# Kernel optimization log

Hardware: AMD Instinct MI355X
Metric: run time of the kernel (lower is better)

## Reference

```python
import jax, jax.numpy as jnp
import numpy as np
import math

MH_C = 2.0 / (math.sqrt(3.0) * math.pi ** 0.25)  # mexican hat normalization

def setup_inputs() -> dict:
    key = jax.random.key(0)
    ks = jax.random.split(key, 4)
    B, O, I, H, W = 4, 32, 32, 128, 128
    x = jax.random.normal(ks[0], (B, I, H, W), dtype=jnp.float32)
    scale_param = jnp.ones((1, O, I, 1, 1), dtype=jnp.float32)
    translation_param = jax.random.normal(ks[1], (1, O, I, 1, 1), dtype=jnp.float32)
    wavelet_conv_w = jax.random.normal(ks[2], (O, I, 3, 3), dtype=jnp.float32) * (1.0 / math.sqrt(I * 9))
    final_conv_w = jax.random.normal(ks[3], (O, O, 1, 1), dtype=jnp.float32) * (1.0 / math.sqrt(O))
    return {"x": x, "scale_param": scale_param, "translation_param": translation_param,
            "wavelet_conv_w": wavelet_conv_w, "final_conv_w": final_conv_w}

def reference(x, scale_param, translation_param, wavelet_conv_w, final_conv_w):
    # x: (B, I, H, W) -> scaled: (B, O, I, H, W)
    sx = (x[:, None] - translation_param) / scale_param
    # mexican hat wavelet, fused elementwise
    wt = MH_C * ((sx * sx - 1.0) * jnp.exp(-0.5 * sx * sx))
    B, O, I, H, W = wt.shape
    # The per-out-channel loop of Conv2d(I,1,k) is exactly a grouped conv with O groups
    wt = wt.reshape(B, O * I, H, W)
    y = jax.lax.conv_general_dilated(
        wt, wavelet_conv_w,
        window_strides=(1, 1), padding=[(1, 1), (1, 1)],
        feature_group_count=O,
        dimension_numbers=("NCHW", "OIHW", "NCHW"))  # (B, O, H, W)
    # final 1x1 conv = channel mix
    out = jnp.einsum("oc,bchw->bohw", final_conv_w[:, :, 0, 0], y)
    return out
```

## Files before the change

kernel.cpp:

```cpp
#include <hip/hip_runtime.h>
#include <math.h>


#define RSTRIP 8

typedef float v2f __attribute__((ext_vector_type(2)));

static __device__ __forceinline__ v2f vfma(float w, v2f a, v2f c) {
  return __builtin_elementwise_fma(a, (v2f){w, w}, c);
}
static __device__ __forceinline__ float bperm(int addr, float v) {
  return __int_as_float(__builtin_amdgcn_ds_bpermute(addr, __float_as_int(v)));
}

#define LDROW(base, r) (*(const v2f*)((base) + (size_t)(min(max((r), 0), 127)) * 128))

__global__ __launch_bounds__(256) void wavelet_grouped_conv(
    const float* __restrict__ x,
    const float* __restrict__ scale,
    const float* __restrict__ trans,
    const float* __restrict__ wconv,
    float* __restrict__ y,
    float mhc)
{
  const int tid   = threadIdx.x;
  const int lane  = tid & 63;
  const int iq    = tid >> 6;
  const int strip = blockIdx.x;
  const int o     = blockIdx.y;
  const int b     = blockIdx.z;
  const int r0    = strip * RSTRIP;
  const int c0    = lane << 1;

  const int a_up = ((lane + 63) & 63) << 2;
  const int a_dn = ((lane +  1) & 63) << 2;
  const bool lane0  = (lane == 0);
  const bool lane63 = (lane == 63);

  const float rvm1 = (r0 > 0)       ? 1.f : 0.f;
  const float rv8  = (r0 + 8 < 128) ? 1.f : 0.f;

  const float NHL2E = -0.72134752044448170f;

  v2f TL[RSTRIP], TC[RSTRIP], TR[RSTRIP];
#pragma unroll
  for (int r = 0; r < RSTRIP; ++r) {
    TL[r] = (v2f){0.f, 0.f}; TC[r] = (v2f){0.f, 0.f}; TR[r] = (v2f){0.f, 0.f};
  }

  const float* xb = x + (size_t)b * 32 * 128 * 128;

#pragma unroll 1
  for (int ii = 0; ii < 8; ++ii) {
    const int i0 = iq * 8 + ii;
    const int oi = __builtin_amdgcn_readfirstlane(o * 32 + i0);
    const float rs  = 1.0f / scale[oi];
    const float trs = trans[oi] * rs;
    const float* wp = wconv + oi * 9;
    const float w00 = wp[0], w01 = wp[1], w02 = wp[2];
    const float w10 = wp[3], w11 = wp[4], w12 = wp[5];
    const float w20 = wp[6], w21 = wp[7], w22 = wp[8];
    const float* base = xb + (size_t)i0 * 128 * 128 + c0;

    v2f xa = LDROW(base, r0 - 1);
    v2f xbv = LDROW(base, r0);

#pragma unroll
    for (int j = 0; j < RSTRIP + 2; ++j) {
      const v2f xc = LDROW(base, r0 + j + 1);
      const float rv = (j == 0) ? rvm1 : (j == RSTRIP + 1) ? rv8 : 1.f;
      const v2f sx = __builtin_elementwise_fma(xa, (v2f){rs, rs},
                                               (v2f){-trs, -trs});
      const v2f u  = sx * sx;
      v2f e;
      e.x = __builtin_amdgcn_exp2f(u.x * NHL2E);
      e.y = __builtin_amdgcn_exp2f(u.y * NHL2E);
      v2f p = __builtin_elementwise_fma(u, (v2f){mhc, mhc},
                                        (v2f){-mhc, -mhc}) * e;
      p = p * (v2f){rv, rv};

      if (j <= RSTRIP - 1) {
        TL[j] = vfma(w00, p, TL[j]);
        TC[j] = vfma(w01, p, TC[j]);
        TR[j] = vfma(w02, p, TR[j]);
      }
      if (j >= 1 && j <= RSTRIP) {
        TL[j-1] = vfma(w10, p, TL[j-1]);
        TC[j-1] = vfma(w11, p, TC[j-1]);
        TR[j-1] = vfma(w12, p, TR[j-1]);
      }
      if (j >= 2) {
        TL[j-2] = vfma(w20, p, TL[j-2]);
        TC[j-2] = vfma(w21, p, TC[j-2]);
        TR[j-2] = vfma(w22, p, TR[j-2]);
      }
      xa = xbv; xbv = xc;
    }
  }

  v2f acc[RSTRIP];
#pragma unroll
  for (int r = 0; r < RSTRIP; ++r) {
    float pl = bperm(a_up, TL[r].y);
    float pr = bperm(a_dn, TR[r].x);
    if (lane0)  pl = 0.f;
    if (lane63) pr = 0.f;
    v2f v;
    v.x = pl      + TC[r].x + TR[r].y;
    v.y = TL[r].x + TC[r].y + pr;
    acc[r] = v;
  }

  __shared__ v2f red[3][RSTRIP][64];
  if (iq != 0) {
#pragma unroll
    for (int r = 0; r < RSTRIP; ++r) red[iq - 1][r][lane] = acc[r];
  }
  __syncthreads();
  if (iq == 0) {
    float* yb = y + (((size_t)b * 32 + o) * 128 + r0) * 128 + c0;
#pragma unroll
    for (int r = 0; r < RSTRIP; ++r) {
      const v2f v = acc[r] + red[0][r][lane] + red[1][r][lane] + red[2][r][lane];
      *(v2f*)(yb + (size_t)r * 128) = v;
    }
  }
}

__global__ __launch_bounds__(256) void mix1x1(
    const float* __restrict__ y,
    const float* __restrict__ fw,
    float* __restrict__ out)
{
  const int px = blockIdx.x * 256 + threadIdx.x;
  const int b  = blockIdx.y;
  const float* yb = y + (size_t)b * 32 * 16384 + px;
  float v[32];
#pragma unroll
  for (int o = 0; o < 32; ++o) v[o] = yb[(size_t)o * 16384];
  float* ob = out + (size_t)b * 32 * 16384 + px;
#pragma unroll
  for (int p = 0; p < 32; ++p) {
    float a = 0.f;
#pragma unroll
    for (int o = 0; o < 32; ++o) a = fmaf(fw[p * 32 + o], v[o], a);
    ob[(size_t)p * 16384] = a;
  }
}

extern "C" void kernel_launch(void* const* d_in, const int* in_sizes, int n_in,
                              void* d_out, int out_size, void* d_ws, size_t ws_size,
                              hipStream_t stream) {
  const float* x     = (const float*)d_in[0];
  const float* scale = (const float*)d_in[1];
  const float* trans = (const float*)d_in[2];
  const float* wconv = (const float*)d_in[3];
  const float* fw    = (const float*)d_in[4];
  float* out = (float*)d_out;
  float* y   = (float*)d_ws;

  const float mhc = (float)(2.0 / (sqrt(3.0) * pow(M_PI, 0.25)));

  dim3 g1(128 / RSTRIP, 32, 4);
  wavelet_grouped_conv<<<g1, 256, 0, stream>>>(x, scale, trans, wconv, y, mhc);

  dim3 g2(16384 / 256, 4);
  mix1x1<<<g2, 256, 0, stream>>>(y, fw, out);
}
```

Before: 46.04 us.

## Double-buffer input rows across channels to prefetch next channel's loads

The per-channel loop now preloads all rows for the next input channel into a second register buffer while computing the current channel, ping-ponging between two buffers across a two-channel unrolled loop. The goal is to hide global load latency behind the exp/FMA work. It also folds the boundary-row mask into the wavelet normalization constant, which saves one multiply per row. The cost is higher register pressure, which may reduce occupancy, plus one redundant clamped load past the last channel.

```diff
diff --git a/kernel.cpp b/kernel.cpp
--- a/kernel.cpp
+++ b/kernel.cpp
@@ -11,6 +11,15 @@
 }
 static __device__ __forceinline__ float bperm(int addr, float v) {
   return __int_as_float(__builtin_amdgcn_ds_bpermute(addr, __float_as_int(v)));
+}
+static __device__ __forceinline__ v2f psi2(v2f xv, float rs, float trs, float m) {
+  const float NHL2E = -0.72134752044448170f;
+  const v2f sx = __builtin_elementwise_fma(xv, (v2f){rs, rs}, (v2f){-trs, -trs});
+  const v2f u  = sx * sx;
+  v2f e;
+  e.x = __builtin_amdgcn_exp2f(u.x * NHL2E);
+  e.y = __builtin_amdgcn_exp2f(u.y * NHL2E);
+  return __builtin_elementwise_fma(u, (v2f){m, m}, (v2f){-m, -m}) * e;
 }
 
 #define LDROW(base, r) (*(const v2f*)((base) + (size_t)(min(max((r), 0), 127)) * 128))
@@ -37,10 +46,8 @@
   const bool lane0  = (lane == 0);
   const bool lane63 = (lane == 63);
 
-  const float rvm1 = (r0 > 0)       ? 1.f : 0.f;
-  const float rv8  = (r0 + 8 < 128) ? 1.f : 0.f;
-
-  const float NHL2E = -0.72134752044448170f;
+  const float mhc_m1 = (r0 > 0)       ? mhc : 0.f;
+  const float mhc_p8 = (r0 + 8 < 128) ? mhc : 0.f;
 
   v2f TL[RSTRIP], TC[RSTRIP], TR[RSTRIP];
 #pragma unroll
@@ -49,54 +56,58 @@
   }
 
   const float* xb = x + (size_t)b * 32 * 128 * 128;
+  const int oibase = __builtin_amdgcn_readfirstlane(o * 32 + iq * 8);
+
+#define CHBASE(k) (xb + (size_t)(min(iq * 8 + (k), 31)) * 128 * 128 + c0)
+
+#define CHANNEL(BUF, NBUF, K)                                               \
+  {                                                                         \
+    const int oi = oibase + (K);                                            \
+    const float rs  = 1.0f / scale[oi];                                     \
+    const float trs = trans[oi] * rs;                                       \
+    const float* wp = wconv + oi * 9;                                       \
+    const float w00 = wp[0], w01 = wp[1], w02 = wp[2];                      \
+    const float w10 = wp[3], w11 = wp[4], w12 = wp[5];                      \
+    const float w20 = wp[6], w21 = wp[7], w22 = wp[8];                      \
+    const float* nb = CHBASE((K) + 1);                                      \
+    _Pragma("unroll")                                                       \
+    for (int k = 0; k < RSTRIP + 2; ++k) NBUF[k] = LDROW(nb, r0 + k - 1);   \
+    _Pragma("unroll")                                                       \
+    for (int j = 0; j < RSTRIP + 2; ++j) {                                  \
+      const float mj = (j == 0) ? mhc_m1 : (j == RSTRIP + 1) ? mhc_p8 : mhc;\
+      const v2f p = psi2(BUF[j], rs, trs, mj);                              \
+      if (j <= RSTRIP - 1) {                                                \
+        TL[j] = vfma(w00, p, TL[j]);                                        \
+        TC[j] = vfma(w01, p, TC[j]);                                        \
+        TR[j] = vfma(w02, p, TR[j]);                                        \
+      }                                                                     \
+      if (j >= 1 && j <= RSTRIP) {                                          \
+        TL[j-1] = vfma(w10, p, TL[j-1]);                                    \
+        TC[j-1] = vfma(w11, p, TC[j-1]);                                    \
+        TR[j-1] = vfma(w12, p, TR[j-1]);                                    \
+      }                                                                     \
+      if (j >= 2) {                                                         \
+        TL[j-2] = vfma(w20, p, TL[j-2]);                                    \
+        TC[j-2] = vfma(w21, p, TC[j-2]);                                    \
+        TR[j-2] = vfma(w22, p, TR[j-2]);                                    \
+      }                                                                     \
+    }                                                                       \
+  }
+
+  v2f bufA[RSTRIP + 2], bufB[RSTRIP + 2];
+  {
+    const float* b0 = CHBASE(0);
+#pragma unroll
+    for (int k = 0; k < RSTRIP + 2; ++k) bufA[k] = LDROW(b0, r0 + k - 1);
+  }
 
 #pragma unroll 1
-  for (int ii = 0; ii < 8; ++ii) {
-    const int i0 = iq * 8 + ii;
-    const int oi = __builtin_amdgcn_readfirstlane(o * 32 + i0);
-    const float rs  = 1.0f / scale[oi];
-    const float trs = trans[oi] * rs;
-    const float* wp = wconv + oi * 9;
-    const float w00 = wp[0], w01 = wp[1], w02 = wp[2];
-    const float w10 = wp[3], w11 = wp[4], w12 = wp[5];
-    const float w20 = wp[6], w21 = wp[7], w22 = wp[8];
-    const float* base = xb + (size_t)i0 * 128 * 128 + c0;
-
-    v2f xa = LDROW(base, r0 - 1);
-    v2f xbv = LDROW(base, r0);
-
-#pragma unroll
-    for (int j = 0; j < RSTRIP + 2; ++j) {
-      const v2f xc = LDROW(base, r0 + j + 1);
-      const float rv = (j == 0) ? rvm1 : (j == RSTRIP + 1) ? rv8 : 1.f;
-      const v2f sx = __builtin_elementwise_fma(xa, (v2f){rs, rs},
-                                               (v2f){-trs, -trs});
-      const v2f u  = sx * sx;
-      v2f e;
-      e.x = __builtin_amdgcn_exp2f(u.x * NHL2E);
-      e.y = __builtin_amdgcn_exp2f(u.y * NHL2E);
-      v2f p = __builtin_elementwise_fma(u, (v2f){mhc, mhc},
-                                        (v2f){-mhc, -mhc}) * e;
-      p = p * (v2f){rv, rv};
-
-      if (j <= RSTRIP - 1) {
-        TL[j] = vfma(w00, p, TL[j]);
-        TC[j] = vfma(w01, p, TC[j]);
-        TR[j] = vfma(w02, p, TR[j]);
-      }
-      if (j >= 1 && j <= RSTRIP) {
-        TL[j-1] = vfma(w10, p, TL[j-1]);
-        TC[j-1] = vfma(w11, p, TC[j-1]);
-        TR[j-1] = vfma(w12, p, TR[j-1]);
-      }
-      if (j >= 2) {
-        TL[j-2] = vfma(w20, p, TL[j-2]);
-        TC[j-2] = vfma(w21, p, TC[j-2]);
-        TR[j-2] = vfma(w22, p, TR[j-2]);
-      }
-      xa = xbv; xbv = xc;
-    }
+  for (int ii = 0; ii < 4; ++ii) {
+    CHANNEL(bufA, bufB, 2 * ii)
+    CHANNEL(bufB, bufA, 2 * ii + 1)
   }
+#undef CHANNEL
+#undef CHBASE
 
   v2f acc[RSTRIP];
 #pragma unroll
```

Result: slower. 48.45 us (+5.2%).

## Split block work across two output channels and halve the row strip

Applied to the files above, without the earlier changes.

Each 256-thread block now handles two output channels, with two waves per channel each covering 16 input channels, instead of one channel with four waves over 8 inputs each. The row strip shrinks from 8 to 4, and row offsets are precomputed so all rows of a channel are loaded up front. The wavelet math is refolded so the scale, exp2 constant, normalisation and boundary masking sit inside per-row coefficients, which removes several multiplies per element. This gives longer per-wave input loops and a smaller reduction, at the cost of more redundant halo-row transcendentals from the shorter strip and a higher launch count.

```diff
diff --git a/kernel.cpp b/kernel.cpp
--- a/kernel.cpp
+++ b/kernel.cpp
@@ -2,7 +2,7 @@
 #include <math.h>
 
 
-#define RSTRIP 8
+#define RSTRIP 4
 
 typedef float v2f __attribute__((ext_vector_type(2)));
 
@@ -12,8 +12,6 @@
 static __device__ __forceinline__ float bperm(int addr, float v) {
   return __int_as_float(__builtin_amdgcn_ds_bpermute(addr, __float_as_int(v)));
 }
-
-#define LDROW(base, r) (*(const v2f*)((base) + (size_t)(min(max((r), 0), 127)) * 128))
 
 __global__ __launch_bounds__(256) void wavelet_grouped_conv(
     const float* __restrict__ x,
@@ -25,10 +23,13 @@
 {
   const int tid   = threadIdx.x;
   const int lane  = tid & 63;
-  const int iq    = tid >> 6;
+  const int wv    = tid >> 6;
+  const int o_idx = wv & 1;
+  const int ihalf = wv >> 1;
   const int strip = blockIdx.x;
-  const int o     = blockIdx.y;
+  const int op    = blockIdx.y;
   const int b     = blockIdx.z;
+  const int o     = op * 2 + o_idx;
   const int r0    = strip * RSTRIP;
   const int c0    = lane << 1;
 
@@ -37,10 +38,14 @@
   const bool lane0  = (lane == 0);
   const bool lane63 = (lane == 63);
 
-  const float rvm1 = (r0 > 0)       ? 1.f : 0.f;
-  const float rv8  = (r0 + 8 < 128) ? 1.f : 0.f;
-
-  const float NHL2E = -0.72134752044448170f;
+  const float C2 = 0.72134752044448170f;
+  const float CC = 0.84932214f;
+  const float K1 = -mhc / C2;
+  const float K2 = -mhc;
+  const float rv0 = (r0 > 0) ? 1.f : 0.f;
+  const float rv5 = (r0 + RSTRIP < 128) ? 1.f : 0.f;
+  const float K1a = K1 * rv0, K2a = K2 * rv0;
+  const float K1b = K1 * rv5, K2b = K2 * rv5;
 
   v2f TL[RSTRIP], TC[RSTRIP], TR[RSTRIP];
 #pragma unroll
@@ -48,37 +53,44 @@
     TL[r] = (v2f){0.f, 0.f}; TC[r] = (v2f){0.f, 0.f}; TR[r] = (v2f){0.f, 0.f};
   }
 
-  const float* xb = x + (size_t)b * 32 * 128 * 128;
+  int off[RSTRIP + 2];
+#pragma unroll
+  for (int j = 0; j < RSTRIP + 2; ++j) {
+    const int row = min(max(r0 + j - 1, 0), 127);
+    off[j] = row * 128 + c0;
+  }
+
+  const float* xb = x + (size_t)b * 32 * 16384;
 
 #pragma unroll 1
-  for (int ii = 0; ii < 8; ++ii) {
-    const int i0 = iq * 8 + ii;
-    const int oi = __builtin_amdgcn_readfirstlane(o * 32 + i0);
-    const float rs  = 1.0f / scale[oi];
-    const float trs = trans[oi] * rs;
+  for (int ci = 0; ci < 16; ++ci) {
+    const int ch = ihalf * 16 + ci;
+    const int oi = __builtin_amdgcn_readfirstlane(o * 32 + ch);
+    const float rsc  = CC / scale[oi];
+    const float trsc = trans[oi] * rsc;
     const float* wp = wconv + oi * 9;
     const float w00 = wp[0], w01 = wp[1], w02 = wp[2];
     const float w10 = wp[3], w11 = wp[4], w12 = wp[5];
     const float w20 = wp[6], w21 = wp[7], w22 = wp[8];
-    const float* base = xb + (size_t)i0 * 128 * 128 + c0;
+    const float* chb = xb + (size_t)ch * 16384;
 
-    v2f xa = LDROW(base, r0 - 1);
-    v2f xbv = LDROW(base, r0);
+    v2f xr[RSTRIP + 2];
+#pragma unroll
+    for (int j = 0; j < RSTRIP + 2; ++j)
+      xr[j] = *(const v2f*)(chb + off[j]);
 
 #pragma unroll
     for (int j = 0; j < RSTRIP + 2; ++j) {
-      const v2f xc = LDROW(base, r0 + j + 1);
-      const float rv = (j == 0) ? rvm1 : (j == RSTRIP + 1) ? rv8 : 1.f;
-      const v2f sx = __builtin_elementwise_fma(xa, (v2f){rs, rs},
-                                               (v2f){-trs, -trs});
-      const v2f u  = sx * sx;
+      const float k1 = (j == 0) ? K1a : (j == RSTRIP + 1) ? K1b : K1;
+      const float k2 = (j == 0) ? K2a : (j == RSTRIP + 1) ? K2b : K2;
+      const v2f v = __builtin_elementwise_fma(xr[j], (v2f){rsc, rsc},
+                                              (v2f){-trsc, -trsc});
+      const v2f wq = -(v * v);
       v2f e;
-      e.x = __builtin_amdgcn_exp2f(u.x * NHL2E);
-      e.y = __builtin_amdgcn_exp2f(u.y * NHL2E);
-      v2f p = __builtin_elementwise_fma(u, (v2f){mhc, mhc},
-                                        (v2f){-mhc, -mhc}) * e;
-      p = p * (v2f){rv, rv};
-
+      e.x = __builtin_amdgcn_exp2f(wq.x);
+      e.y = __builtin_amdgcn_exp2f(wq.y);
+      const v2f p = __builtin_elementwise_fma(wq, (v2f){k1, k1},
+                                              (v2f){k2, k2}) * e;
       if (j <= RSTRIP - 1) {
         TL[j] = vfma(w00, p, TL[j]);
         TC[j] = vfma(w01, p, TC[j]);
@@ -94,7 +106,6 @@
         TC[j-2] = vfma(w21, p, TC[j-2]);
         TR[j-2] = vfma(w22, p, TR[j-2]);
       }
-      xa = xbv; xbv = xc;
     }
   }
 
@@ -111,17 +122,17 @@
     acc[r] = v;
   }
 
-  __shared__ v2f red[3][RSTRIP][64];
-  if (iq != 0) {
+  __shared__ v2f red[2][RSTRIP][64];
+  if (ihalf == 1) {
 #pragma unroll
-    for (int r = 0; r < RSTRIP; ++r) red[iq - 1][r][lane] = acc[r];
+    for (int r = 0; r < RSTRIP; ++r) red[o_idx][r][lane] = acc[r];
   }
   __syncthreads();
-  if (iq == 0) {
+  if (ihalf == 0) {
     float* yb = y + (((size_t)b * 32 + o) * 128 + r0) * 128 + c0;
 #pragma unroll
     for (int r = 0; r < RSTRIP; ++r) {
-      const v2f v = acc[r] + red[0][r][lane] + red[1][r][lane] + red[2][r][lane];
+      const v2f v = acc[r] + red[o_idx][r][lane];
       *(v2f*)(yb + (size_t)r * 128) = v;
     }
   }
@@ -161,7 +172,7 @@
 
   const float mhc = (float)(2.0 / (sqrt(3.0) * pow(M_PI, 0.25)));
 
-  dim3 g1(128 / RSTRIP, 32, 4);
+  dim3 g1(128 / RSTRIP, 16, 4);
   wavelet_grouped_conv<<<g1, 256, 0, stream>>>(x, scale, trans, wconv, y, mhc);
 
   dim3 g2(16384 / 256, 4);
```

New measurement: 47.14 us. +2.4%, slower.

## Use packed fp16 dot2 for conv taps and fold wavelet constants into exp2

Applied to the files above, without the earlier changes.

The grouped conv now processes input channels in pairs. Wavelet values are packed to fp16 and each tap is accumulated with fdot2, which roughly halves the FMA count. The wavelet maths is reformulated so the exp2 argument needs no extra multiply, and the boundary-row masks are folded into the polynomial constants. Row offsets are precomputed instead of reloading via a rolling window. The 1x1 mix kernel is also split across two grid slices of output channels for more parallelism. The cost is fp16 rounding of weights and activations, which lowers accuracy.

```diff
diff --git a/kernel.cpp b/kernel.cpp
--- a/kernel.cpp
+++ b/kernel.cpp
@@ -5,15 +5,11 @@
 #define RSTRIP 8
 
 typedef float v2f __attribute__((ext_vector_type(2)));
+typedef __fp16 h2 __attribute__((ext_vector_type(2)));
 
-static __device__ __forceinline__ v2f vfma(float w, v2f a, v2f c) {
-  return __builtin_elementwise_fma(a, (v2f){w, w}, c);
-}
 static __device__ __forceinline__ float bperm(int addr, float v) {
   return __int_as_float(__builtin_amdgcn_ds_bpermute(addr, __float_as_int(v)));
 }
-
-#define LDROW(base, r) (*(const v2f*)((base) + (size_t)(min(max((r), 0), 127)) * 128))
 
 __global__ __launch_bounds__(256) void wavelet_grouped_conv(
     const float* __restrict__ x,
@@ -37,10 +33,14 @@
   const bool lane0  = (lane == 0);
   const bool lane63 = (lane == 63);
 
-  const float rvm1 = (r0 > 0)       ? 1.f : 0.f;
-  const float rv8  = (r0 + 8 < 128) ? 1.f : 0.f;
-
-  const float NHL2E = -0.72134752044448170f;
+  const float C2 = 0.72134752044448170f;
+  const float CC = 0.84932214f;
+  const float K1 = -mhc / C2;
+  const float K2 = -mhc;
+  const float rv0 = (r0 > 0) ? 1.f : 0.f;
+  const float rv9 = (r0 + RSTRIP < 128) ? 1.f : 0.f;
+  const float K1a = K1 * rv0, K2a = K2 * rv0;
+  const float K1b = K1 * rv9, K2b = K2 * rv9;
 
   v2f TL[RSTRIP], TC[RSTRIP], TR[RSTRIP];
 #pragma unroll
@@ -48,53 +48,77 @@
     TL[r] = (v2f){0.f, 0.f}; TC[r] = (v2f){0.f, 0.f}; TR[r] = (v2f){0.f, 0.f};
   }
 
-  const float* xb = x + (size_t)b * 32 * 128 * 128;
+  int off[RSTRIP + 2];
+#pragma unroll
+  for (int j = 0; j < RSTRIP + 2; ++j) {
+    const int row = min(max(r0 + j - 1, 0), 127);
+    off[j] = row * 128 + c0;
+  }
+
+  const float* xb = x + (size_t)b * 32 * 16384;
 
 #pragma unroll 1
-  for (int ii = 0; ii < 8; ++ii) {
-    const int i0 = iq * 8 + ii;
-    const int oi = __builtin_amdgcn_readfirstlane(o * 32 + i0);
-    const float rs  = 1.0f / scale[oi];
-    const float trs = trans[oi] * rs;
-    const float* wp = wconv + oi * 9;
-    const float w00 = wp[0], w01 = wp[1], w02 = wp[2];
-    const float w10 = wp[3], w11 = wp[4], w12 = wp[5];
-    const float w20 = wp[6], w21 = wp[7], w22 = wp[8];
-    const float* base = xb + (size_t)i0 * 128 * 128 + c0;
-
-    v2f xa = LDROW(base, r0 - 1);
-    v2f xbv = LDROW(base, r0);
+  for (int pr = 0; pr < 4; ++pr) {
+    const int chA = iq * 8 + 2 * pr;
+    const int oiA = __builtin_amdgcn_readfirstlane(o * 32 + chA);
+    const int oiB = oiA + 1;
+    const float rscA  = CC / scale[oiA];
+    const float trscA = trans[oiA] * rscA;
+    const float rscB  = CC / scale[oiB];
+    const float trscB = trans[oiB] * rscB;
+    const float* wpA = wconv + oiA * 9;
+    const float* wpB = wconv + oiB * 9;
+    h2 wpk[9];
+#pragma unroll
+    for (int k = 0; k < 9; ++k)
+      wpk[k] = __builtin_amdgcn_cvt_pkrtz(wpA[k], wpB[k]);
+    const float* baseA = xb + (size_t)chA * 16384;
+    const float* baseB = baseA + 16384;
 
 #pragma unroll
     for (int j = 0; j < RSTRIP + 2; ++j) {
-      const v2f xc = LDROW(base, r0 + j + 1);
-      const float rv = (j == 0) ? rvm1 : (j == RSTRIP + 1) ? rv8 : 1.f;
-      const v2f sx = __builtin_elementwise_fma(xa, (v2f){rs, rs},
-                                               (v2f){-trs, -trs});
-      const v2f u  = sx * sx;
-      v2f e;
-      e.x = __builtin_amdgcn_exp2f(u.x * NHL2E);
-      e.y = __builtin_amdgcn_exp2f(u.y * NHL2E);
-      v2f p = __builtin_elementwise_fma(u, (v2f){mhc, mhc},
-                                        (v2f){-mhc, -mhc}) * e;
-      p = p * (v2f){rv, rv};
+      const float k1 = (j == 0) ? K1a : (j == RSTRIP + 1) ? K1b : K1;
+      const float k2 = (j == 0) ? K2a : (j == RSTRIP + 1) ? K2b : K2;
+      const v2f xA = *(const v2f*)(baseA + off[j]);
+      const v2f xB = *(const v2f*)(baseB + off[j]);
+      const v2f vA = __builtin_elementwise_fma(xA, (v2f){rscA, rscA},
+                                               (v2f){-trscA, -trscA});
+      const v2f vB = __builtin_elementwise_fma(xB, (v2f){rscB, rscB},
+                                               (v2f){-trscB, -trscB});
+      const v2f wqA = -(vA * vA);
+      const v2f wqB = -(vB * vB);
+      v2f eA, eB;
+      eA.x = __builtin_amdgcn_exp2f(wqA.x);
+      eA.y = __builtin_amdgcn_exp2f(wqA.y);
+      eB.x = __builtin_amdgcn_exp2f(wqB.x);
+      eB.y = __builtin_amdgcn_exp2f(wqB.y);
+      const v2f gA = __builtin_elementwise_fma(wqA, (v2f){k1, k1},
+                                               (v2f){k2, k2}) * eA;
+      const v2f gB = __builtin_elementwise_fma(wqB, (v2f){k1, k1},
+                                               (v2f){k2, k2}) * eB;
+      const h2 px = __builtin_amdgcn_cvt_pkrtz(gA.x, gB.x);
+      const h2 py = __builtin_amdgcn_cvt_pkrtz(gA.y, gB.y);
+
+#define TAP2(ACC, WK)                                                 \
+      ACC.x = __builtin_amdgcn_fdot2(WK, px, ACC.x, false);           \
+      ACC.y = __builtin_amdgcn_fdot2(WK, py, ACC.y, false);
 
       if (j <= RSTRIP - 1) {
-        TL[j] = vfma(w00, p, TL[j]);
-        TC[j] = vfma(w01, p, TC[j]);
-        TR[j] = vfma(w02, p, TR[j]);
+        TAP2(TL[j], wpk[0])
+        TAP2(TC[j], wpk[1])
+        TAP2(TR[j], wpk[2])
       }
       if (j >= 1 && j <= RSTRIP) {
-        TL[j-1] = vfma(w10, p, TL[j-1]);
-        TC[j-1] = vfma(w11, p, TC[j-1]);
-        TR[j-1] = vfma(w12, p, TR[j-1]);
+        TAP2(TL[j-1], wpk[3])
+        TAP2(TC[j-1], wpk[4])
+        TAP2(TR[j-1], wpk[5])
       }
       if (j >= 2) {
-        TL[j-2] = vfma(w20, p, TL[j-2]);
-        TC[j-2] = vfma(w21, p, TC[j-2]);
-        TR[j-2] = vfma(w22, p, TR[j-2]);
+        TAP2(TL[j-2], wpk[6])
+        TAP2(TC[j-2], wpk[7])
+        TAP2(TR[j-2], wpk[8])
       }
-      xa = xbv; xbv = xc;
+#undef TAP2
     }
   }
 
@@ -134,17 +158,19 @@
 {
   const int px = blockIdx.x * 256 + threadIdx.x;
   const int b  = blockIdx.y;
+  const int ph = blockIdx.z;
   const float* yb = y + (size_t)b * 32 * 16384 + px;
   float v[32];
 #pragma unroll
   for (int o = 0; o < 32; ++o) v[o] = yb[(size_t)o * 16384];
   float* ob = out + (size_t)b * 32 * 16384 + px;
 #pragma unroll
-  for (int p = 0; p < 32; ++p) {
+  for (int p = 0; p < 16; ++p) {
+    const int po = ph * 16 + p;
     float a = 0.f;
 #pragma unroll
-    for (int o = 0; o < 32; ++o) a = fmaf(fw[p * 32 + o], v[o], a);
-    ob[(size_t)p * 16384] = a;
+    for (int o = 0; o < 32; ++o) a = fmaf(fw[po * 32 + o], v[o], a);
+    ob[(size_t)po * 16384] = a;
   }
 }
 
@@ -164,6 +190,6 @@
   dim3 g1(128 / RSTRIP, 32, 4);
   wavelet_grouped_conv<<<g1, 256, 0, stream>>>(x, scale, trans, wconv, y, mhc);
 
-  dim3 g2(16384 / 256, 4);
+  dim3 g2(16384 / 256, 4, 2);
   mix1x1<<<g2, 256, 0, stream>>>(y, fw, out);
 }
```

New measurement: 48.83 us. +6.1%, slower.
